# Kernel tuning notes

Measured on AMD Instinct MI355X. Metric: run time of the kernel, lower is better.

The kernel has to match this reference:

```python
import jax, jax.numpy as jnp
import numpy as np

OUT, IN, V, K, R = 4096, 4096, 8, 4096, 128
TOKENS = 8192

def setup_inputs() -> dict:
    key = jax.random.key(0)
    ks = jax.random.split(key, 9)
    return {
        "x": jax.random.normal(ks[0], (TOKENS, IN), dtype=jnp.float32),
        "centroids": jax.random.normal(ks[1], (K, V), dtype=jnp.float32),
        "indices": jax.random.randint(ks[2], (OUT, IN // V), 0, K, dtype=jnp.int32),
        "U": jax.random.normal(ks[3], (OUT, R), dtype=jnp.float32) * 0.02,
        "S": jax.random.uniform(ks[4], (R,), dtype=jnp.float32) + 0.1,
        "Vt": jax.random.normal(ks[5], (R, IN), dtype=jnp.float32) * 0.02,
        "weight_scale": jax.random.uniform(ks[6], (OUT,), dtype=jnp.float32) + 0.5,
        "weight_bias": jax.random.normal(ks[7], (OUT,), dtype=jnp.float32) * 0.01,
        "bias": jax.random.normal(ks[8], (OUT,), dtype=jnp.float32),
    }

def dequant_weight(centroids, indices, U, S, Vt, weight_scale, weight_bias):
    # codebook lookup: [OUT, IN//V] indices -> [OUT, IN//V, V] -> [OUT, IN]
    w_q = centroids[indices].reshape(indices.shape[0], -1)
    # per-output-channel affine
    w_q = w_q * weight_scale[:, None] + weight_bias[:, None]
    # low-rank SVD correction: U @ diag(S) @ Vt
    lowrank = jnp.einsum('or,r,ri->oi', U, S, Vt)
    return w_q + lowrank

def reference(x, centroids, indices, U, S, Vt, weight_scale, weight_bias, bias):
    dtype = x.dtype
    weight = dequant_weight(centroids, indices, U, S, Vt, weight_scale, weight_bias)
    # result = x @ W^T + bias  (as in forward)
    result = x @ weight.T.astype(dtype) + bias.astype(dtype)[None, :]
    return result.astype(dtype)
```

## Files before the change

### kernel.cpp

```cpp
#include <hip/hip_runtime.h>
#include <hip/hip_bf16.h>
#include <stdint.h>

using bf16 = __hip_bfloat16;
typedef __bf16 bf16x8 __attribute__((ext_vector_type(8)));
typedef float f32x4 __attribute__((ext_vector_type(4)));
typedef short short8 __attribute__((ext_vector_type(8)));

#define GLD_LDS16(gp, lp)                                                            \
  __builtin_amdgcn_global_load_lds(                                                  \
      (const __attribute__((address_space(1))) unsigned int*)(gp),                   \
      (__attribute__((address_space(3))) unsigned int*)(lp), 16, 0, 0)

__global__ __launch_bounds__(256) void prep_convert(const float* __restrict__ x,
                                                    bf16* __restrict__ xb, int n,
                                                    const float* __restrict__ U,
                                                    const float* __restrict__ S,
                                                    const float* __restrict__ Vt,
                                                    bf16* __restrict__ Ub,
                                                    bf16* __restrict__ SVtT)
{
  __shared__ float tile[64][65];
  const int b = blockIdx.x;
  const int t = threadIdx.x;

  if (b < 128) {
    const int i0 = (b >> 1) * 64;
    const int r0 = (b & 1) * 64;
    const int lrow = t >> 4;
    const int lcol = (t & 15) * 4;
#pragma unroll
    for (int p = 0; p < 4; p++) {
      const int row = p * 16 + lrow;
      const float s = S[r0 + row];
      const float4 v = *(const float4*)(Vt + (size_t)(r0 + row) * 4096 + i0 + lcol);
      tile[row][lcol + 0] = v.x * s;
      tile[row][lcol + 1] = v.y * s;
      tile[row][lcol + 2] = v.z * s;
      tile[row][lcol + 3] = v.w * s;
    }
    __syncthreads();
    const int il = t >> 2;
    const int rq = (t & 3) * 16;
    union { bf16 h[16]; short8 v[2]; } u;
#pragma unroll
    for (int j = 0; j < 16; j++)
      u.h[j] = __float2bfloat16(tile[rq + j][il]);
    short8* dst = (short8*)(SVtT + (size_t)(i0 + il) * 128 + r0 + rq);
    dst[0] = u.v[0];
    dst[1] = u.v[1];
  } else if (b < 384) {
    const int i = ((b - 128) * 256 + t) * 8;
    float4 a0 = *(const float4*)(U + i);
    float4 a1 = *(const float4*)(U + i + 4);
    union { bf16 h[8]; short8 v; } u;
    u.h[0] = __float2bfloat16(a0.x); u.h[1] = __float2bfloat16(a0.y);
    u.h[2] = __float2bfloat16(a0.z); u.h[3] = __float2bfloat16(a0.w);
    u.h[4] = __float2bfloat16(a1.x); u.h[5] = __float2bfloat16(a1.y);
    u.h[6] = __float2bfloat16(a1.z); u.h[7] = __float2bfloat16(a1.w);
    *(short8*)(Ub + i) = u.v;
  } else {
    const int vb = b - 384;
    for (int i = (vb * 256 + t) * 16; i < n; i += 2048 * 256 * 16) {
      float4 a = *(const float4*)(x + i);
      float4 c = *(const float4*)(x + i + 4);
      float4 d = *(const float4*)(x + i + 8);
      float4 e = *(const float4*)(x + i + 12);
      union { bf16 h[16]; short8 v[2]; } u;
      u.h[0]  = __float2bfloat16(a.x); u.h[1]  = __float2bfloat16(a.y);
      u.h[2]  = __float2bfloat16(a.z); u.h[3]  = __float2bfloat16(a.w);
      u.h[4]  = __float2bfloat16(c.x); u.h[5]  = __float2bfloat16(c.y);
      u.h[6]  = __float2bfloat16(c.z); u.h[7]  = __float2bfloat16(c.w);
      u.h[8]  = __float2bfloat16(d.x); u.h[9]  = __float2bfloat16(d.y);
      u.h[10] = __float2bfloat16(d.z); u.h[11] = __float2bfloat16(d.w);
      u.h[12] = __float2bfloat16(e.x); u.h[13] = __float2bfloat16(e.y);
      u.h[14] = __float2bfloat16(e.z); u.h[15] = __float2bfloat16(e.w);
      *(short8*)(xb + i)     = u.v[0];
      *(short8*)(xb + i + 8) = u.v[1];
    }
  }
}

__global__ __launch_bounds__(256, 2) void gemm_wbuild(const bf16* __restrict__ A,
                                                      const bf16* __restrict__ B,
                                                      bf16* __restrict__ Cb,
                                                      int M, int N, int K,
                                                      const int* __restrict__ indices,
                                                      const float* __restrict__ centroids,
                                                      const float* __restrict__ wscale,
                                                      const float* __restrict__ wbias)
{
  __shared__ bf16 As4[4 * 4096];
  __shared__ bf16 Bs4[4 * 4096];

  const int tid  = threadIdx.x;
  const int m0   = blockIdx.y * 128;
  const int n0   = blockIdx.x * 128;
  const int wid  = tid >> 6;
  const int lane = tid & 63;
  const int wm   = wid >> 1;
  const int wn   = wid & 1;
  const int kk   = (lane >> 4) * 8;
  const int fr   = lane & 15;

  const int sr = tid >> 2;
  const int sc = (tid & 3) * 8;
  const bf16* ga = A + (size_t)(m0 + sr) * 128 + sc;
  const bf16* gb = B + (size_t)(n0 + sr) * 128 + sc;

#pragma unroll
  for (int c = 0; c < 4; c++) {
    GLD_LDS16(ga + 32 * c,            &As4[c * 4096 + tid * 8]);
    GLD_LDS16(ga + 32 * c + 64 * 128, &As4[c * 4096 + 2048 + tid * 8]);
    GLD_LDS16(gb + 32 * c,            &Bs4[c * 4096 + tid * 8]);
    GLD_LDS16(gb + 32 * c + 64 * 128, &Bs4[c * 4096 + 2048 + tid * 8]);
  }
  __syncthreads();

  f32x4 acc[4][4] = {};
#pragma unroll
  for (int c = 0; c < 4; c++) {
    bf16x8 af[4], bfr[4];
#pragma unroll
    for (int m = 0; m < 4; m++)
      af[m] = *(const bf16x8*)(&As4[c * 4096 + (wm * 64 + m * 16 + fr) * 32 + kk]);
#pragma unroll
    for (int n = 0; n < 4; n++)
      bfr[n] = *(const bf16x8*)(&Bs4[c * 4096 + (wn * 64 + n * 16 + fr) * 32 + kk]);
#pragma unroll
    for (int m = 0; m < 4; m++)
#pragma unroll
      for (int n = 0; n < 4; n++)
        acc[m][n] = __builtin_amdgcn_mfma_f32_16x16x32_bf16(af[m], bfr[n], acc[m][n], 0, 0, 0);
  }

#pragma unroll
  for (int m = 0; m < 4; m++) {
#pragma unroll
    for (int n = 0; n < 4; n++) {
      const int col  = n0 + wn * 64 + n * 16 + (lane & 15);
      const int rowb = m0 + wm * 64 + m * 16 + (lane >> 4) * 4;
#pragma unroll
      for (int j = 0; j < 4; j++) {
        const int row  = rowb + j;
        const int idxv = indices[row * 512 + (col >> 3)];
        const float cv = centroids[idxv * 8 + (col & 7)];
        const float w  = cv * wscale[row] + wbias[row] + acc[m][n][j];
        Cb[(size_t)row * N + col] = __float2bfloat16(w);
      }
    }
  }
}

__global__ __launch_bounds__(512, 2) void gemm256(const bf16* __restrict__ A,
                                                  const bf16* __restrict__ B,
                                                  float* __restrict__ C,
                                                  const float* __restrict__ bias)
{
  extern __shared__ char smem[];
  constexpr int K = 4096;
  constexpr int N = 4096;

  const int tid  = threadIdx.x;
  const int lane = tid & 63;
  const int wave = tid >> 6;
  const int wm   = wave >> 2;
  const int wn   = wave & 3;
  const int fr   = lane & 15;
  const int kk   = (lane >> 4) * 8;
  const int swx  = (fr & 7) << 4;

  const int bid = blockIdx.x;
  const int xcd = bid & 7;
  const int idx = bid >> 3;
  const int mi  = (xcd & 3) * 8 + (idx & 7);
  const int ni  = (xcd >> 2) * 8 + (idx >> 3);
  const int m0  = mi * 256;
  const int n0  = ni * 256;

  const int pA = tid * 16;
  const int rA = pA >> 7;
  const int kA = ((pA ^ ((rA & 7) << 4)) & 127) >> 1;
  const bf16* gA0 = A + (size_t)(m0 + rA) * K + kA;
  const int pB = (tid >> 8) * 8192 + (tid & 255) * 16;
  const int rB = pB >> 7;
  const int kB = ((pB ^ ((rB & 7) << 4)) & 127) >> 1;
  const bf16* gB0 = B + (size_t)(n0 + rB) * K + kB;

  f32x4 acc[8][4] = {};

  const int laneK0 = fr * 128 + ((kk * 2) ^ swx);
  const int laneK1 = fr * 128 + ((64 + kk * 2) ^ swx);
  const char* bA00 = smem + wm * 16384 + laneK0;
  const char* bA01 = smem + wm * 16384 + laneK1;
  const char* bA10 = bA00 + 65536;
  const char* bA11 = bA01 + 65536;
  const char* bB00 = smem + 32768 + wn * 8192 + laneK0;
  const char* bB01 = smem + 32768 + wn * 8192 + laneK1;
  const char* bB10 = bB00 + 65536;
  const char* bB11 = bB01 + 65536;

#define STG_A0(bo) GLD_LDS16(gA_p,                   smem + (bo) + pA)
#define STG_A1(bo) GLD_LDS16(gA_p + 128 * 4096,      smem + (bo) + pA + 16384)
#define STG_A2(bo) GLD_LDS16(gA_p +  64 * 4096,      smem + (bo) + pA + 8192)
#define STG_A3(bo) GLD_LDS16(gA_p + 192 * 4096,      smem + (bo) + pA + 24576)
#define STG_B0(bo) GLD_LDS16(gB_p,                   smem + (bo) + 32768 + pB)
#define STG_B1(bo) GLD_LDS16(gB_p + 128 * 4096,      smem + (bo) + 32768 + pB + 16384)
#define STG_B2(bo) GLD_LDS16(gB_p + 64 +  32 * 4096, smem + (bo) + 32768 + pB + 4096)
#define STG_B3(bo) GLD_LDS16(gB_p + 64 + 160 * 4096, smem + (bo) + 32768 + pB + 20480)

#define LOAD_AQ(dst, qm, P0, P1)                                                    \
  _Pragma("unroll") for (int mm = 0; mm < 4; mm++)                                  \
    _Pragma("unroll") for (int ks = 0; ks < 2; ks++)                                \
      dst[mm][ks] = *(const bf16x8*)((ks ? (P1) : (P0)) +                           \
                                     ((qm) * 8192 + mm * 2048));

#define LOAD_BQ(dst, qn, P0, P1)                                                    \
  _Pragma("unroll") for (int nn = 0; nn < 2; nn++)                                  \
    _Pragma("unroll") for (int ks = 0; ks < 2; ks++)                                \
      dst[nn][ks] = *(const bf16x8*)((ks ? (P1) : (P0)) +                           \
                                     ((qn) * 4096 + nn * 2048));

#define CLUSTER(qm, qn, av, bv)                                                     \
  __builtin_amdgcn_s_setprio(1);                                                    \
  _Pragma("unroll") for (int ks = 0; ks < 2; ks++)                                  \
    _Pragma("unroll") for (int mm = 0; mm < 4; mm++)                                \
      _Pragma("unroll") for (int nn = 0; nn < 2; nn++)                              \
        acc[(qm) * 4 + mm][(qn) * 2 + nn] =                                         \
            __builtin_amdgcn_mfma_f32_16x16x32_bf16(                                \
                av[mm][ks], bv[nn][ks], acc[(qm) * 4 + mm][(qn) * 2 + nn],          \
                0, 0, 0);                                                           \
  __builtin_amdgcn_s_setprio(0);

#define SBAR   __builtin_amdgcn_s_barrier()
#define SCHED0 __builtin_amdgcn_sched_barrier(0)
#define VM4    asm volatile("s_waitcnt vmcnt(4)" ::: "memory")

  bf16x8 aq0[4][2], aq1[4][2], b0[2][2], b1[2][2], b0r[2][2];

  GLD_LDS16(gA0,                  smem + pA);
  GLD_LDS16(gA0 + 128 * 4096,     smem + pA + 16384);
  GLD_LDS16(gB0,                  smem + 32768 + pB);
  GLD_LDS16(gB0 + 128 * 4096,     smem + 32768 + pB + 16384);
  GLD_LDS16(gB0 +  32 * 4096,     smem + 32768 + pB + 4096);
  GLD_LDS16(gB0 + 160 * 4096,     smem + 32768 + pB + 20480);
  GLD_LDS16(gA0 +  64 * 4096,     smem + pA + 8192);
  GLD_LDS16(gA0 + 192 * 4096,     smem + pA + 24576);
  GLD_LDS16(gA0 + 64,             smem + 65536 + pA);
  GLD_LDS16(gA0 + 64 + 128 * 4096, smem + 65536 + pA + 16384);
  GLD_LDS16(gB0 + 64 +  32 * 4096, smem + 65536 + 32768 + pB + 4096);
  GLD_LDS16(gB0 + 64 + 160 * 4096, smem + 65536 + 32768 + pB + 20480);
  GLD_LDS16(gA0 + 64 +  64 * 4096, smem + 65536 + pA + 8192);
  GLD_LDS16(gA0 + 64 + 192 * 4096, smem + 65536 + pA + 24576);
  asm volatile("s_waitcnt vmcnt(6)" ::: "memory");
  SBAR;
  LOAD_AQ(aq0, 0, bA00, bA01);
  LOAD_BQ(b0, 0, bB00, bB01);
  SCHED0;

  const bf16* gA_p = gA0 + 128;
  const bf16* gB_p = gB0 + 64;

#define TILE(AB, NB, ABa0, ABa1, ABb0, ABb1, NBa0, NBa1, NBb0, NBb1)                \
  {                                                                                 \
                    \
    SBAR;                                                                           \
    STG_B0(NB); STG_B1(NB);                                                         \
    LOAD_BQ(b1, 1, ABb0, ABb1);                                                     \
    SCHED0;                                                                         \
    CLUSTER(0, 0, aq0, b0);                                                         \
    SCHED0;                                                                         \
                  \
    SBAR;                                                                           \
    STG_A0(AB); STG_A1(AB);                                                         \
    SCHED0;                                                                         \
    CLUSTER(0, 1, aq0, b1);                                                         \
    SCHED0;                                                                         \
    LOAD_AQ(aq1, 1, ABa0, ABa1);                                                    \
    SCHED0;                                                                         \
                   \
    SBAR;                                                                           \
    STG_B2(AB); STG_B3(AB);                                                         \
    LOAD_BQ(b0r, 0, ABb0, ABb1);                                                    \
    SCHED0;                                                                         \
    CLUSTER(1, 1, aq1, b1);                                                         \
    SCHED0;                                                                         \
    \
    VM4;                                                                            \
    SBAR;                                                                           \
    STG_A2(AB); STG_A3(AB);                                                         \
    SCHED0;                                                                         \
    CLUSTER(1, 0, aq1, b0r);                                                        \
    SCHED0;                                                                         \
    LOAD_AQ(aq0, 0, NBa0, NBa1);                                                    \
    LOAD_BQ(b0, 0, NBb0, NBb1);                                                     \
    SCHED0;                                                                         \
    gA_p += 64; gB_p += 64;                                                         \
  }

  for (int tt = 0; tt < 32; tt++) {
    TILE(0, 65536, bA00, bA01, bB00, bB01, bA10, bA11, bB10, bB11);
    TILE(65536, 0, bA10, bA11, bB10, bB11, bA00, bA01, bB00, bB01);
  }

#pragma unroll
  for (int mf = 0; mf < 8; mf++) {
#pragma unroll
    for (int nf = 0; nf < 4; nf++) {
      const int col  = n0 + wn * 64 + nf * 16 + fr;
      const int row0 = m0 + wm * 128 + mf * 16 + (lane >> 4) * 4;
      const float bv = bias[col];
#pragma unroll
      for (int j = 0; j < 4; j++)
        C[(size_t)(row0 + j) * N + col] = acc[mf][nf][j] + bv;
    }
  }
#undef TILE
#undef CLUSTER
#undef LOAD_AQ
#undef LOAD_BQ
#undef SBAR
#undef SCHED0
#undef VM4
#undef STG_A0
#undef STG_A1
#undef STG_A2
#undef STG_A3
#undef STG_B0
#undef STG_B1
#undef STG_B2
#undef STG_B3
}

extern "C" void kernel_launch(void* const* d_in, const int* in_sizes, int n_in,
                              void* d_out, int out_size, void* d_ws, size_t ws_size,
                              hipStream_t stream)
{
  const float* x         = (const float*)d_in[0];
  const float* centroids = (const float*)d_in[1];
  const int*   indices   = (const int*)d_in[2];
  const float* U         = (const float*)d_in[3];
  const float* S         = (const float*)d_in[4];
  const float* Vt        = (const float*)d_in[5];
  const float* wscale    = (const float*)d_in[6];
  const float* wbias     = (const float*)d_in[7];
  const float* bias      = (const float*)d_in[8];
  float* out = (float*)d_out;

  char* ws = (char*)d_ws;
  bf16* xb   = (bf16*)(ws);
  bf16* Wb   = (bf16*)(ws + 67108864);
  bf16* Ub   = (bf16*)(ws + 100663296);
  bf16* SVtT = (bf16*)(ws + 101711872);

  prep_convert<<<2432, 256, 0, stream>>>(x, xb, 8192 * 4096, U, S, Vt, Ub, SVtT);

  dim3 gW(4096 / 128, 4096 / 128);
  gemm_wbuild<<<gW, 256, 0, stream>>>(Ub, SVtT, Wb, 4096, 4096, 128,
                                      indices, centroids, wscale, wbias);

  gemm256<<<512, 512, 131072, stream>>>(xb, Wb, out, bias);
}
```

Baseline: 280.8 us.

## Restructure GEMM main loop into explicit phases with lgkm waits and double barriers

Reworks the software-pipelined bf16 GEMM main loop. LDS fragment loads now happen at the start of each phase, followed by explicit lgkmcnt waits and a barrier on both sides of each MFMA cluster. The global-to-LDS staging is reordered to match, with vmcnt(6) waits in place of vmcnt(4). The intent is a cleaner producer/consumer schedule, but the extra barriers and full lgkm drains per phase may serialize LDS reads against MFMA work that was previously overlapped.

```diff
diff --git a/kernel.cpp b/kernel.cpp
--- a/kernel.cpp
+++ b/kernel.cpp
@@ -200,14 +200,14 @@
   const char* bB10 = bB00 + 65536;
   const char* bB11 = bB01 + 65536;
 
-#define STG_A0(bo) GLD_LDS16(gA_p,                   smem + (bo) + pA)
-#define STG_A1(bo) GLD_LDS16(gA_p + 128 * 4096,      smem + (bo) + pA + 16384)
-#define STG_A2(bo) GLD_LDS16(gA_p +  64 * 4096,      smem + (bo) + pA + 8192)
-#define STG_A3(bo) GLD_LDS16(gA_p + 192 * 4096,      smem + (bo) + pA + 24576)
-#define STG_B0(bo) GLD_LDS16(gB_p,                   smem + (bo) + 32768 + pB)
-#define STG_B1(bo) GLD_LDS16(gB_p + 128 * 4096,      smem + (bo) + 32768 + pB + 16384)
-#define STG_B2(bo) GLD_LDS16(gB_p + 64 +  32 * 4096, smem + (bo) + 32768 + pB + 4096)
-#define STG_B3(bo) GLD_LDS16(gB_p + 64 + 160 * 4096, smem + (bo) + 32768 + pB + 20480)
+#define SA0(g, bo) GLD_LDS16((g),              smem + (bo) + pA)
+#define SA1(g, bo) GLD_LDS16((g) + 128 * 4096, smem + (bo) + pA + 16384)
+#define SA2(g, bo) GLD_LDS16((g) +  64 * 4096, smem + (bo) + pA + 8192)
+#define SA3(g, bo) GLD_LDS16((g) + 192 * 4096, smem + (bo) + pA + 24576)
+#define SB0(g, bo) GLD_LDS16((g),              smem + (bo) + 32768 + pB)
+#define SB1(g, bo) GLD_LDS16((g) + 128 * 4096, smem + (bo) + 32768 + pB + 16384)
+#define SB2(g, bo) GLD_LDS16((g) +  32 * 4096, smem + (bo) + 32768 + pB + 4096)
+#define SB3(g, bo) GLD_LDS16((g) + 160 * 4096, smem + (bo) + 32768 + pB + 20480)
 
 #define LOAD_AQ(dst, qm, P0, P1)                                                    \
   _Pragma("unroll") for (int mm = 0; mm < 4; mm++)                                  \
@@ -234,73 +234,62 @@
 
 #define SBAR   __builtin_amdgcn_s_barrier()
 #define SCHED0 __builtin_amdgcn_sched_barrier(0)
-#define VM4    asm volatile("s_waitcnt vmcnt(4)" ::: "memory")
+#define LG0    asm volatile("s_waitcnt lgkmcnt(0)" ::: "memory")
+#define LG8    asm volatile("s_waitcnt lgkmcnt(8)" ::: "memory")
+#define VM6    asm volatile("s_waitcnt vmcnt(6)" ::: "memory")
+
+#define PH_TAIL(qm, qn, av, bv)                                                     \
+  SBAR; LG0; SCHED0; CLUSTER(qm, qn, av, bv); SBAR; SCHED0;
 
   bf16x8 aq0[4][2], aq1[4][2], b0[2][2], b1[2][2], b0r[2][2];
 
-  GLD_LDS16(gA0,                  smem + pA);
-  GLD_LDS16(gA0 + 128 * 4096,     smem + pA + 16384);
-  GLD_LDS16(gB0,                  smem + 32768 + pB);
-  GLD_LDS16(gB0 + 128 * 4096,     smem + 32768 + pB + 16384);
-  GLD_LDS16(gB0 +  32 * 4096,     smem + 32768 + pB + 4096);
-  GLD_LDS16(gB0 + 160 * 4096,     smem + 32768 + pB + 20480);
-  GLD_LDS16(gA0 +  64 * 4096,     smem + pA + 8192);
-  GLD_LDS16(gA0 + 192 * 4096,     smem + pA + 24576);
-  GLD_LDS16(gA0 + 64,             smem + 65536 + pA);
-  GLD_LDS16(gA0 + 64 + 128 * 4096, smem + 65536 + pA + 16384);
-  GLD_LDS16(gB0 + 64 +  32 * 4096, smem + 65536 + 32768 + pB + 4096);
-  GLD_LDS16(gB0 + 64 + 160 * 4096, smem + 65536 + 32768 + pB + 20480);
-  GLD_LDS16(gA0 + 64 +  64 * 4096, smem + 65536 + pA + 8192);
-  GLD_LDS16(gA0 + 64 + 192 * 4096, smem + 65536 + pA + 24576);
-  asm volatile("s_waitcnt vmcnt(6)" ::: "memory");
+  SA0(gA0, 0); SA1(gA0, 0);
+  SB0(gB0, 0); SB1(gB0, 0);
+  SB2(gB0, 0); SB3(gB0, 0);
+  SA2(gA0, 0); SA3(gA0, 0);
+  SA0(gA0 + 64, 65536); SA1(gA0 + 64, 65536);
+  SB2(gB0 + 64, 65536); SB3(gB0 + 64, 65536);
+  SA2(gA0 + 64, 65536); SA3(gA0 + 64, 65536);
+  VM6;
   SBAR;
-  LOAD_AQ(aq0, 0, bA00, bA01);
-  LOAD_BQ(b0, 0, bB00, bB01);
   SCHED0;
 
   const bf16* gA_p = gA0 + 128;
   const bf16* gB_p = gB0 + 64;
 
-#define TILE(AB, NB, ABa0, ABa1, ABb0, ABb1, NBa0, NBa1, NBb0, NBb1)                \
-  {                                                                                 \
-                    \
-    SBAR;                                                                           \
-    STG_B0(NB); STG_B1(NB);                                                         \
-    LOAD_BQ(b1, 1, ABb0, ABb1);                                                     \
-    SCHED0;                                                                         \
-    CLUSTER(0, 0, aq0, b0);                                                         \
-    SCHED0;                                                                         \
-                  \
-    SBAR;                                                                           \
-    STG_A0(AB); STG_A1(AB);                                                         \
-    SCHED0;                                                                         \
-    CLUSTER(0, 1, aq0, b1);                                                         \
-    SCHED0;                                                                         \
-    LOAD_AQ(aq1, 1, ABa0, ABa1);                                                    \
-    SCHED0;                                                                         \
-                   \
-    SBAR;                                                                           \
-    STG_B2(AB); STG_B3(AB);                                                         \
-    LOAD_BQ(b0r, 0, ABb0, ABb1);                                                    \
-    SCHED0;                                                                         \
-    CLUSTER(1, 1, aq1, b1);                                                         \
-    SCHED0;                                                                         \
-    \
-    VM4;                                                                            \
-    SBAR;                                                                           \
-    STG_A2(AB); STG_A3(AB);                                                         \
-    SCHED0;                                                                         \
-    CLUSTER(1, 0, aq1, b0r);                                                        \
-    SCHED0;                                                                         \
-    LOAD_AQ(aq0, 0, NBa0, NBa1);                                                    \
-    LOAD_BQ(b0, 0, NBb0, NBb1);                                                     \
-    SCHED0;                                                                         \
-    gA_p += 64; gB_p += 64;                                                         \
-  }
-
   for (int tt = 0; tt < 32; tt++) {
-    TILE(0, 65536, bA00, bA01, bB00, bB01, bA10, bA11, bB10, bB11);
-    TILE(65536, 0, bA10, bA11, bB10, bB11, bA00, bA01, bB00, bB01);
+    LOAD_AQ(aq0, 0, bA00, bA01);
+    LOAD_BQ(b0, 0, bB00, bB01);
+    SB0(gB_p, 65536); SB1(gB_p, 65536);
+    LG8;
+    PH_TAIL(0, 0, aq0, b0);
+    LOAD_BQ(b1, 1, bB00, bB01);
+    SA0(gA_p, 0); SA1(gA_p, 0);
+    PH_TAIL(0, 1, aq0, b1);
+    LOAD_AQ(aq1, 1, bA00, bA01);
+    SB2(gB_p + 64, 0); SB3(gB_p + 64, 0);
+    PH_TAIL(1, 1, aq1, b1);
+    LOAD_BQ(b0r, 0, bB00, bB01);
+    SA2(gA_p, 0); SA3(gA_p, 0);
+    VM6;
+    PH_TAIL(1, 0, aq1, b0r);
+    LOAD_AQ(aq0, 0, bA10, bA11);
+    LOAD_BQ(b0, 0, bB10, bB11);
+    SB0(gB_p + 64, 0); SB1(gB_p + 64, 0);
+    LG8;
+    PH_TAIL(0, 0, aq0, b0);
+    LOAD_BQ(b1, 1, bB10, bB11);
+    SA0(gA_p + 64, 65536); SA1(gA_p + 64, 65536);
+    PH_TAIL(0, 1, aq0, b1);
+    LOAD_AQ(aq1, 1, bA10, bA11);
+    SB2(gB_p + 128, 65536); SB3(gB_p + 128, 65536);
+    PH_TAIL(1, 1, aq1, b1);
+    LOAD_BQ(b0r, 0, bB10, bB11);
+    SA2(gA_p + 64, 65536); SA3(gA_p + 64, 65536);
+    VM6;
+    PH_TAIL(1, 0, aq1, b0r);
+
+    gA_p += 128; gB_p += 128;
   }
 
 #pragma unroll
@@ -315,21 +304,23 @@
         C[(size_t)(row0 + j) * N + col] = acc[mf][nf][j] + bv;
     }
   }
-#undef TILE
+#undef PH_TAIL
 #undef CLUSTER
 #undef LOAD_AQ
 #undef LOAD_BQ
 #undef SBAR
 #undef SCHED0
-#undef VM4
-#undef STG_A0
-#undef STG_A1
-#undef STG_A2
-#undef STG_A3
-#undef STG_B0
-#undef STG_B1
-#undef STG_B2
-#undef STG_B3
+#undef LG0
+#undef LG8
+#undef VM6
+#undef SA0
+#undef SA1
+#undef SA2
+#undef SA3
+#undef SB0
+#undef SB1
+#undef SB2
+#undef SB3
 }
 
 extern "C" void kernel_launch(void* const* d_in, const int* in_sizes, int n_in,
```

Result: slower. 291.7 us (+3.9%).
